# Kernel tuning notes

Hardware: AMD Instinct MI355X
Metric: run time of the kernel (lower is better)

## Reference

```python
import jax, jax.numpy as jnp
import numpy as np

# --- model dimensions ---
MAX_UP = 512; MAX_DOWN = 512; MAX_ELEC = MAX_UP + MAX_DOWN  # 1024 orbitals
N_NUC = 128
MAX_CHARGE = 16
TOT_ORB = MAX_CHARGE * (MAX_CHARGE + 1) // 2  # 136
NUM_HEADS = 8; D_HEAD = 32; F = NUM_HEADS * D_HEAD  # 256
L = 4          # num_layers
FN = 256       # nuc_feats dim
SIGMOID_SHIFTS = (2.0, 4.0, 6.0)
E_DIM = 3 + 1 + len(SIGMOID_SHIFTS)  # featurized edge dim = 7


def generate_spd_orbitals(charges):
    """Vectorized form of the scan/fori_loop scatter in the source.
    For nucleus n with charge c: orbitals[cum_charge+i, n, c(c-1)/2+i] = 1 for i<c.
    charges: [N_NUC] int. Returns [MAX_ELEC, N_NUC, TOT_ORB] float32."""
    c = charges.astype(jnp.int32)
    off = jnp.cumsum(c) - c                      # exclusive cumsum (cum_charge)
    prec = c * (c - 1) // 2                      # preceding orbital offset
    i = jnp.arange(MAX_CHARGE, dtype=jnp.int32)
    valid = (i[None, :] < c[:, None])            # [N_NUC, MAX_CHARGE]
    elec = jnp.clip(off[:, None] + i[None, :], 0, MAX_ELEC - 1)
    orbi = jnp.clip(prec[:, None] + i[None, :], 0, TOT_ORB - 1)
    nuc = jnp.broadcast_to(jnp.arange(N_NUC, dtype=jnp.int32)[:, None], (N_NUC, MAX_CHARGE))
    orb = jnp.zeros((MAX_ELEC, N_NUC, TOT_ORB), jnp.float32)
    return orb.at[elec.ravel(), nuc.ravel(), orbi.ravel()].add(valid.ravel().astype(jnp.float32))


def make_permutation(n_up, n_down):
    segments = [0, n_up, MAX_UP, MAX_UP + n_down, MAX_ELEC]
    updates = [0, n_down, -MAX_UP + n_up, 0]
    idx = jnp.arange(MAX_ELEC)
    agg = jnp.zeros_like(idx)
    for lft, r, u in zip(segments[:-1], segments[1:], updates):
        agg = agg + ((idx >= lft) & (idx < r)) * (idx + u)
    return agg


def featurize_real_space_vector(diffs):
    """[N,N,3] -> [N,N,7]: rescaled diffs, log1p(|r|), sigmoid(|r|-shift)."""
    norm = jnp.sqrt(jnp.sum(diffs * diffs, -1, keepdims=True) + 1e-12)
    sig = jnp.concatenate([jax.nn.sigmoid(norm - s) for s in SIGMOID_SHIFTS], -1)
    return jnp.concatenate([diffs / (1.0 + norm), jnp.log1p(norm), sig], -1)


def orb_ln(x):
    """OrbLayerNorm(feat_axis=-1, nuc_axis=1, eps=1.0) on [O, N, F] tensors."""
    mean = jnp.mean(x, -1, keepdims=True)
    var = jnp.var(x, -1, keepdims=True)
    max_var = jnp.max(var, axis=1, keepdims=True)
    return jax.lax.rsqrt(max_var + 1.0) * (x - mean)


def setup_inputs() -> dict:
    key = jax.random.key(0)
    ks = jax.random.split(key, 8)
    coords = jax.random.normal(ks[0], (N_NUC, 3), jnp.float32) * 3.0
    charges = jax.random.randint(ks[1], (N_NUC,), 0, 8)  # sum < MAX_ELEC
    nuc_mask = jnp.ones((N_NUC,), bool)
    nuc_feats = jax.random.normal(ks[2], (N_NUC, FN), jnp.float32)
    orb_mask = jnp.ones((MAX_ELEC,), bool)
    # hk.Linear(num_feats, with_bias=False, TruncatedNormal(stddev=1))
    W_orb = jax.random.truncated_normal(ks[3], -2.0, 2.0, (TOT_ORB, F), jnp.float32)
    W_edge = jax.random.normal(ks[4], (L, E_DIM, NUM_HEADS), jnp.float32) / np.sqrt(E_DIM)
    W_val = jax.random.normal(ks[5], (L, F, F), jnp.float32) / np.sqrt(F)
    W_nuc = jax.random.normal(ks[6], (L, FN, F), jnp.float32) / np.sqrt(FN)
    W_out = jax.random.normal(ks[7], (L, F, F), jnp.float32) / np.sqrt(F)
    return dict(coords=coords, charges=charges, nuc_mask=nuc_mask, n_up=500,
                n_down=480, nuc_feats=nuc_feats, orb_mask=orb_mask, W_orb=W_orb,
                W_edge=W_edge, W_val=W_val, W_nuc=W_nuc, W_out=W_out)


def reference(coords, charges, nuc_mask, n_up, n_down, nuc_feats, orb_mask,
              W_orb, W_edge, W_val, W_nuc, W_out):
    orbital_feats = generate_spd_orbitals(charges)               # [O, N, TOT_ORB]
    perm = make_permutation(int(n_up), int(n_down))
    orbital_feats = orbital_feats[perm]
    feats = jnp.einsum('ont,tf->onf', orbital_feats, W_orb)     # [O, N, F]
    m = (orb_mask[:, None, None] & nuc_mask[None, :, None]).astype(feats.dtype)
    feats = feats * m
    diffs = coords[:, None, :] - coords[None, :, :]              # [N, N, 3]
    nn_mask = nuc_mask[:, None] & nuc_mask[None, :]
    edge = featurize_real_space_vector(diffs) * nn_mask[..., None]  # [N, N, E]
    for l in range(L):
        # --- MaskedMPNNBlock ---
        h = orb_ln(feats)
        vals = jnp.einsum('onf,fg->ong', h, W_val[l]).reshape(MAX_ELEC, N_NUC, NUM_HEADS, D_HEAD)
        ew = jnp.einsum('ije,eh->ijh', edge, W_edge[l]) * nn_mask[..., None]
        msg = jnp.einsum('ijh,ojhd->oihd', ew, vals).reshape(MAX_ELEC, N_NUC, F)
        msg = msg + nuc_feats @ W_nuc[l]
        feats = feats + jnp.einsum('onf,fg->ong', jnp.tanh(orb_ln(msg)), W_out[l])
        feats = feats * m
    return feats
```

## Files before the change

### kernel.cpp

```cpp
#include <hip/hip_runtime.h>
#include <hip/hip_bf16.h>


#define O_TOT 1024

typedef __bf16 bf16x8 __attribute__((ext_vector_type(8)));
typedef float f32x4 __attribute__((ext_vector_type(4)));

static __device__ __forceinline__ unsigned short f2bf(float f) {
  __bf16 b = (__bf16)f;
  unsigned short u;
  __builtin_memcpy(&u, &b, 2);
  return u;
}
static __device__ __forceinline__ float ftanh(float x) {
  float e = __expf(2.f * x);
  return 1.f - 2.f * __builtin_amdgcn_rcpf(e + 1.f);
}

struct alignas(8) US4 { unsigned short a, b, c, d; };

static __device__ __forceinline__ int swzA(int row, int cb) {
  return row * 512 + (cb ^ ((row & 7) << 4) ^ (((row >> 3) & 1) << 5));
}
static __device__ __forceinline__ int swzV(int row, int cb) {
  return row * 256 + (cb ^ ((row & 7) << 4) ^ (((row >> 3) & 1) << 5));
}


__global__ void k_orbmap(const int* __restrict__ charges, const int* __restrict__ n_up_p,
                         const int* __restrict__ n_down_p, int* __restrict__ orb_nuc,
                         int* __restrict__ orb_t) {
  __shared__ int off[129];
  __shared__ int prec[128];
  int tid = threadIdx.x;
  if (tid == 0) {
    int a = 0;
    for (int n = 0; n < 128; ++n) { off[n] = a; a += charges[n]; }
    off[128] = a;
  }
  if (tid < 128) prec[tid] = charges[tid] * (charges[tid] - 1) / 2;
  __syncthreads();
  int nu = *n_up_p, nd = *n_down_p;
  for (int o = tid; o < O_TOT; o += 256) {
    int e;
    if (o < nu) e = o;
    else if (o < 512) e = o + nd;
    else if (o < 512 + nd) e = o + nu - 512;
    else e = o;
    int nn = -1, tt = 0;
    for (int n = 0; n < 128; ++n) {
      if (e >= off[n] && e < off[n + 1]) { nn = n; tt = prec[n] + (e - off[n]); }
    }
    orb_nuc[o] = nn;
    orb_t[o] = tt;
  }
}

__global__ void k_ew(const float* __restrict__ coords, const float* __restrict__ W_edge,
                     unsigned short* __restrict__ ewbf) {
  int i = blockIdx.x, j = threadIdx.x;
  float dx = coords[i * 3 + 0] - coords[j * 3 + 0];
  float dy = coords[i * 3 + 1] - coords[j * 3 + 1];
  float dz = coords[i * 3 + 2] - coords[j * 3 + 2];
  float norm = sqrtf(dx * dx + dy * dy + dz * dz + 1e-12f);
  float inv = 1.f / (1.f + norm);
  float e[7];
  e[0] = dx * inv; e[1] = dy * inv; e[2] = dz * inv;
  e[3] = log1pf(norm);
  e[4] = 1.f / (1.f + expf(-(norm - 2.f)));
  e[5] = 1.f / (1.f + expf(-(norm - 4.f)));
  e[6] = 1.f / (1.f + expf(-(norm - 6.f)));
  const int mt = i >> 4, l16 = i & 15;
  const int k0 = j >> 5, jo = j & 31;
  const int lane = (jo >> 3) * 16 + l16, jj = jo & 7;
  for (int l = 0; l < 4; ++l)
    for (int h = 0; h < 8; ++h) {
      float s = 0.f;
      for (int k = 0; k < 7; ++k) s += e[k] * W_edge[(l * 7 + k) * 8 + h];
      ewbf[(((((l * 8 + h) * 8 + mt) * 4 + k0) * 64) + lane) * 8 + jj] = f2bf(s);
    }
}

__global__ void k_wt(const float* __restrict__ Wv, const float* __restrict__ Wo,
                     unsigned short* __restrict__ WvTf, unsigned short* __restrict__ WoTf) {
  int idx = blockIdx.x * 256 + threadIdx.x;
  const int l = idx >> 16, rem = idx & 65535;
  const int jj = rem & 7, lane = (rem >> 3) & 63, k0 = (rem >> 9) & 7, gt = rem >> 12;
  const int g = gt * 16 + (lane & 15);
  const int f = k0 * 32 + (lane >> 4) * 8 + jj;
  const int src = l * 65536 + f * 256 + g;
  WvTf[idx] = f2bf(Wv[src]);
  WoTf[idx] = f2bf(Wo[src]);
}

__global__ void k_nucbT(const float* __restrict__ nuc_feats, const float* __restrict__ W_nuc,
                        float* __restrict__ nucbT) {
  int b = blockIdx.x;
  int l = b >> 7, i = b & 127;
  int g = threadIdx.x;
  __shared__ float row[256];
  row[g] = nuc_feats[i * 256 + g];
  __syncthreads();
  const float* Wn = W_nuc + l * 65536;
  float s = 0.f;
  for (int f = 0; f < 256; ++f) s += row[f] * Wn[f * 256 + g];
  nucbT[(l * 256 + g) * 128 + i] = s;
}


__global__ __launch_bounds__(512, 2) void k_main(
    float* __restrict__ feats,
    const float* __restrict__ W_orb,
    const unsigned short* __restrict__ WvTf,
    const unsigned short* __restrict__ WoTf,
    const unsigned short* __restrict__ ewbf,
    const float* __restrict__ nucbT,
    const int* __restrict__ orb_nuc, const int* __restrict__ orb_t) {
  __shared__ char SB[65536];
  __shared__ float2 ln2s[8][128];
  __shared__ float red[8];

  const int o = blockIdx.x;
  const int tid = threadIdx.x;
  const int wave = tid >> 6;
  const int lane = tid & 63;
  const int l16 = lane & 15;
  const int kgrp = (lane >> 4) << 3;
  const int rgrp = (lane >> 4) << 2;
  const int w16 = wave * 16;

  const int nn = orb_nuc[o];
  const int tt = orb_t[o];
  float* fo = feats + (size_t)o * 32768;

  f32x4 fr[16];
#pragma unroll
  for (int gt = 0; gt < 16; ++gt) {
    f32x4 v = {0.f, 0.f, 0.f, 0.f};
#pragma unroll
    for (int r = 0; r < 4; ++r)
      if (w16 + rgrp + r == nn) v[r] = W_orb[tt * 256 + gt * 16 + l16];
    fr[gt] = v;
  }

#pragma unroll 1
  for (int l = 0; l < 4; ++l) {
    bf16x8 A[8];
    {
      float s[4] = {0, 0, 0, 0}, q[4] = {0, 0, 0, 0};
#pragma unroll
      for (int gt = 0; gt < 16; ++gt)
#pragma unroll
        for (int r = 0; r < 4; ++r) {
          float v = fr[gt][r];
          s[r] += v; q[r] += v * v;
        }
#pragma unroll
      for (int of = 1; of < 16; of <<= 1)
#pragma unroll
        for (int r = 0; r < 4; ++r) {
          s[r] += __shfl_xor(s[r], of);
          q[r] += __shfl_xor(q[r], of);
        }
      float mean[4], maxv = 0.f;
#pragma unroll
      for (int r = 0; r < 4; ++r) {
        mean[r] = s[r] * (1.f / 256.f);
        const float var = q[r] * (1.f / 256.f) - mean[r] * mean[r];
        maxv = fmaxf(maxv, var);
      }
      maxv = fmaxf(maxv, __shfl_xor(maxv, 16));
      maxv = fmaxf(maxv, __shfl_xor(maxv, 32));
      if (lane == 0) red[wave] = maxv;
#pragma unroll
      for (int gt = 0; gt < 16; ++gt)
#pragma unroll
        for (int r = 0; r < 4; ++r)
          *(unsigned short*)(SB + swzA(w16 + rgrp + r, (gt * 16 + l16) * 2)) =
              f2bf(fr[gt][r] - mean[r]);
#pragma unroll
      for (int k0 = 0; k0 < 8; ++k0)
        A[k0] = *(const bf16x8*)(SB + swzA(w16 + l16, (k0 * 32 + kgrp) * 2));
    }
    __syncthreads();

    {
      float mv = red[0];
#pragma unroll
      for (int w = 1; w < 8; ++w) mv = fmaxf(mv, red[w]);
      const float rstd = rsqrtf(mv + 1.f);
      const unsigned short* Wl = WvTf + (l * 16 * 8 * 64 * 8) + lane * 8;
#pragma unroll
      for (int gt = 0; gt < 16; ++gt) {
        f32x4 acc = {0.f, 0.f, 0.f, 0.f};
        bf16x8 b[4];
#pragma unroll
        for (int k0 = 0; k0 < 4; ++k0)
          b[k0] = *(const bf16x8*)(Wl + (gt * 8 + k0) * 512);
#pragma unroll
        for (int k0 = 0; k0 < 4; ++k0)
          acc = __builtin_amdgcn_mfma_f32_16x16x32_bf16(A[k0], b[k0], acc, 0, 0, 0);
#pragma unroll
        for (int k0 = 0; k0 < 4; ++k0)
          b[k0] = *(const bf16x8*)(Wl + (gt * 8 + k0 + 4) * 512);
#pragma unroll
        for (int k0 = 0; k0 < 4; ++k0)
          acc = __builtin_amdgcn_mfma_f32_16x16x32_bf16(A[k0 + 4], b[k0], acc, 0, 0, 0);
        const int gg = gt * 16 + l16;
        US4 ov{f2bf(acc[0] * rstd), f2bf(acc[1] * rstd), f2bf(acc[2] * rstd),
               f2bf(acc[3] * rstd)};
        *(US4*)(SB + swzV(gg, (w16 + rgrp) * 2)) = ov;
      }
    }
    __syncthreads();

    bf16x8 B0[4], B1[4];
#pragma unroll
    for (int k0 = 0; k0 < 4; ++k0) {
      B0[k0] = *(const bf16x8*)(SB + swzV(wave * 32 + l16, (k0 * 32 + kgrp) * 2));
      B1[k0] = *(const bf16x8*)(SB + swzV(wave * 32 + 16 + l16, (k0 * 32 + kgrp) * 2));
    }
    __syncthreads();

    {
      const unsigned short* ewh = ewbf + ((l * 8 + wave) * 8 * 4 * 64 * 8) + lane * 8;
      const float* nbT = nucbT + l * 32768;
      const int f0 = wave * 32 + l16;
      const int f1 = f0 + 16;
#pragma unroll
      for (int mt = 0; mt < 8; ++mt) {
        const int i0 = mt * 16;
        f32x4 acc0 = {0.f, 0.f, 0.f, 0.f}, acc1 = {0.f, 0.f, 0.f, 0.f};
        {
          bf16x8 a0 = *(const bf16x8*)(ewh + (mt * 4 + 0) * 512);
          bf16x8 a1 = *(const bf16x8*)(ewh + (mt * 4 + 1) * 512);
          acc0 = __builtin_amdgcn_mfma_f32_16x16x32_bf16(a0, B0[0], acc0, 0, 0, 0);
          acc1 = __builtin_amdgcn_mfma_f32_16x16x32_bf16(a0, B1[0], acc1, 0, 0, 0);
          acc0 = __builtin_amdgcn_mfma_f32_16x16x32_bf16(a1, B0[1], acc0, 0, 0, 0);
          acc1 = __builtin_amdgcn_mfma_f32_16x16x32_bf16(a1, B1[1], acc1, 0, 0, 0);
        }
        {
          bf16x8 a0 = *(const bf16x8*)(ewh + (mt * 4 + 2) * 512);
          bf16x8 a1 = *(const bf16x8*)(ewh + (mt * 4 + 3) * 512);
          acc0 = __builtin_amdgcn_mfma_f32_16x16x32_bf16(a0, B0[2], acc0, 0, 0, 0);
          acc1 = __builtin_amdgcn_mfma_f32_16x16x32_bf16(a0, B1[2], acc1, 0, 0, 0);
          acc0 = __builtin_amdgcn_mfma_f32_16x16x32_bf16(a1, B0[3], acc0, 0, 0, 0);
          acc1 = __builtin_amdgcn_mfma_f32_16x16x32_bf16(a1, B1[3], acc1, 0, 0, 0);
        }
        const f32x4 nb0 = *(const f32x4*)(nbT + f0 * 128 + i0 + rgrp);
        const f32x4 nb1 = *(const f32x4*)(nbT + f1 * 128 + i0 + rgrp);
        float sp[4], qp[4];
#pragma unroll
        for (int r = 0; r < 4; ++r) {
          const float v0 = acc0[r] + nb0[r];
          const float v1 = acc1[r] + nb1[r];
          *(unsigned short*)(SB + swzA(i0 + rgrp + r, f0 * 2)) = f2bf(v0);
          *(unsigned short*)(SB + swzA(i0 + rgrp + r, f1 * 2)) = f2bf(v1);
          sp[r] = v0 + v1;
          qp[r] = v0 * v0 + v1 * v1;
        }
#pragma unroll
        for (int of = 1; of < 16; of <<= 1)
#pragma unroll
          for (int r = 0; r < 4; ++r) {
            sp[r] += __shfl_xor(sp[r], of);
            qp[r] += __shfl_xor(qp[r], of);
          }
        if (l16 == 0) {
#pragma unroll
          for (int r = 0; r < 4; ++r)
            ln2s[wave][i0 + rgrp + r] = float2{sp[r], qp[r]};
        }
      }
    }
    __syncthreads();

    {
      float s0 = 0.f, q0 = 0.f, s1v = 0.f, q1v = 0.f;
#pragma unroll
      for (int h = 0; h < 8; ++h) {
        const float2 p0 = ln2s[h][lane];
        const float2 p1 = ln2s[h][lane + 64];
        s0 += p0.x; q0 += p0.y;
        s1v += p1.x; q1v += p1.y;
      }
      const float mean_a = s0 * (1.f / 256.f);
      const float mean_b = s1v * (1.f / 256.f);
      float v0 = q0 * (1.f / 256.f) - mean_a * mean_a;
      float v1 = q1v * (1.f / 256.f) - mean_b * mean_b;
      float mv = fmaxf(v0, v1);
#pragma unroll
      for (int of = 1; of < 64; of <<= 1) mv = fmaxf(mv, __shfl_xor(mv, of));
      const float rstd2 = rsqrtf(mv + 1.f);
      const float meansel = (wave >= 4) ? mean_b : mean_a;
      const float mn = __shfl(meansel, ((wave & 3) << 4) + l16);

      bf16x8 A2[8];
#pragma unroll
      for (int k0 = 0; k0 < 8; ++k0) {
        bf16x8 raw = *(const bf16x8*)(SB + swzA(w16 + l16, (k0 * 32 + kgrp) * 2));
        bf16x8 t;
#pragma unroll
        for (int j = 0; j < 8; ++j)
          t[j] = (__bf16)ftanh(((float)raw[j] - mn) * rstd2);
        A2[k0] = t;
      }

      const unsigned short* Wl = WoTf + (l * 16 * 8 * 64 * 8) + lane * 8;
#pragma unroll
      for (int gt = 0; gt < 16; ++gt) {
        f32x4 acc = fr[gt];
        bf16x8 b[4];
#pragma unroll
        for (int k0 = 0; k0 < 4; ++k0)
          b[k0] = *(const bf16x8*)(Wl + (gt * 8 + k0) * 512);
#pragma unroll
        for (int k0 = 0; k0 < 4; ++k0)
          acc = __builtin_amdgcn_mfma_f32_16x16x32_bf16(A2[k0], b[k0], acc, 0, 0, 0);
#pragma unroll
        for (int k0 = 0; k0 < 4; ++k0)
          b[k0] = *(const bf16x8*)(Wl + (gt * 8 + k0 + 4) * 512);
#pragma unroll
        for (int k0 = 0; k0 < 4; ++k0)
          acc = __builtin_amdgcn_mfma_f32_16x16x32_bf16(A2[k0 + 4], b[k0], acc, 0, 0, 0);
        fr[gt] = acc;
      }
    }
  }

#pragma unroll
  for (int gt = 0; gt < 16; ++gt)
#pragma unroll
    for (int r = 0; r < 4; ++r)
      fo[(w16 + rgrp + r) * 256 + gt * 16 + l16] = fr[gt][r];
}


extern "C" void kernel_launch(void* const* d_in, const int* in_sizes, int n_in,
                              void* d_out, int out_size, void* d_ws, size_t ws_size,
                              hipStream_t stream) {
  const float* coords = (const float*)d_in[0];
  const int* charges = (const int*)d_in[1];
  const int* n_up = (const int*)d_in[3];
  const int* n_down = (const int*)d_in[4];
  const float* nuc_feats = (const float*)d_in[5];
  const float* W_orb = (const float*)d_in[7];
  const float* W_edge = (const float*)d_in[8];
  const float* W_val = (const float*)d_in[9];
  const float* W_nuc = (const float*)d_in[10];
  const float* W_out = (const float*)d_in[11];
  float* out = (float*)d_out;

  char* ws = (char*)d_ws;
  int* orb_nuc = (int*)ws;
  int* orb_t = (int*)(ws + 4096);
  unsigned short* ewbf = (unsigned short*)(ws + 8192);
  unsigned short* WvTf = (unsigned short*)(ws + 8192 + 1048576);
  unsigned short* WoTf = WvTf + 262144;
  float* nucbT = (float*)(ws + 8192 + 1048576 + 1048576);

  k_orbmap<<<dim3(1), dim3(256), 0, stream>>>(charges, n_up, n_down, orb_nuc, orb_t);
  k_ew<<<dim3(128), dim3(128), 0, stream>>>(coords, W_edge, ewbf);
  k_wt<<<dim3(1024), dim3(256), 0, stream>>>(W_val, W_out, WvTf, WoTf);
  k_nucbT<<<dim3(512), dim3(256), 0, stream>>>(nuc_feats, W_nuc, nucbT);
  k_main<<<dim3(O_TOT), dim3(512), 0, stream>>>(out, W_orb, WvTf, WoTf, ewbf, nucbT,
                                                orb_nuc, orb_t);
}
```

Before: 651.2 us.

## Pack residual features to bf16 in AGPRs and raise occupancy to four blocks

The fp32 residual accumulator (64 floats per thread) is replaced with 32 packed bf16 pairs pinned to accumulator registers, and launch bounds rise from 2 to 4 blocks per CU to improve latency hiding. The second layernorm statistics are now computed from the bf16 values read back from LDS, with a per-row reduction, instead of from per-tile shuffles and a shared partial-sum array. Weight loads are interleaved two at a time with the MFMAs to cut live registers. Keeping the residual stream in bf16 loses precision across layers, and 64 KB of LDS per block may still limit how many blocks actually fit per CU.

```diff
diff --git a/kernel.cpp b/kernel.cpp
--- a/kernel.cpp
+++ b/kernel.cpp
@@ -12,6 +12,21 @@
   unsigned short u;
   __builtin_memcpy(&u, &b, 2);
   return u;
+}
+static __device__ __forceinline__ unsigned int packbf(float a, float b) {
+  return (unsigned int)f2bf(a) | ((unsigned int)f2bf(b) << 16);
+}
+static __device__ __forceinline__ float lo16f(unsigned int u) {
+  unsigned int x = u << 16;
+  float f;
+  __builtin_memcpy(&f, &x, 4);
+  return f;
+}
+static __device__ __forceinline__ float hi16f(unsigned int u) {
+  unsigned int x = u & 0xffff0000u;
+  float f;
+  __builtin_memcpy(&f, &x, 4);
+  return f;
 }
 static __device__ __forceinline__ float ftanh(float x) {
   float e = __expf(2.f * x);
@@ -109,7 +124,7 @@
 }
 
 
-__global__ __launch_bounds__(512, 2) void k_main(
+__global__ __launch_bounds__(512, 4) void k_main(
     float* __restrict__ feats,
     const float* __restrict__ W_orb,
     const unsigned short* __restrict__ WvTf,
@@ -118,8 +133,8 @@
     const float* __restrict__ nucbT,
     const int* __restrict__ orb_nuc, const int* __restrict__ orb_t) {
   __shared__ char SB[65536];
-  __shared__ float2 ln2s[8][128];
-  __shared__ float red[8];
+  __shared__ float red1[8];
+  __shared__ float red2[8];
 
   const int o = blockIdx.x;
   const int tid = threadIdx.x;
@@ -134,51 +149,60 @@
   const int tt = orb_t[o];
   float* fo = feats + (size_t)o * 32768;
 
-  f32x4 fr[16];
+  unsigned int frw[32];
 #pragma unroll
   for (int gt = 0; gt < 16; ++gt) {
-    f32x4 v = {0.f, 0.f, 0.f, 0.f};
+    float v[4] = {0.f, 0.f, 0.f, 0.f};
 #pragma unroll
     for (int r = 0; r < 4; ++r)
       if (w16 + rgrp + r == nn) v[r] = W_orb[tt * 256 + gt * 16 + l16];
-    fr[gt] = v;
-  }
+    frw[2 * gt] = packbf(v[0], v[1]);
+    frw[2 * gt + 1] = packbf(v[2], v[3]);
+  }
+#pragma unroll
+  for (int i = 0; i < 32; ++i) asm volatile("" : "+a"(frw[i]));
 
 #pragma unroll 1
   for (int l = 0; l < 4; ++l) {
     bf16x8 A[8];
     {
-      float s[4] = {0, 0, 0, 0}, q[4] = {0, 0, 0, 0};
-#pragma unroll
-      for (int gt = 0; gt < 16; ++gt)
+      float s4[4] = {0, 0, 0, 0}, q4[4] = {0, 0, 0, 0};
+#pragma unroll
+      for (int gt = 0; gt < 16; ++gt) {
+        const float v0 = lo16f(frw[2 * gt]), v1 = hi16f(frw[2 * gt]);
+        const float v2 = lo16f(frw[2 * gt + 1]), v3 = hi16f(frw[2 * gt + 1]);
+        s4[0] += v0; q4[0] += v0 * v0;
+        s4[1] += v1; q4[1] += v1 * v1;
+        s4[2] += v2; q4[2] += v2 * v2;
+        s4[3] += v3; q4[3] += v3 * v3;
+      }
+#pragma unroll
+      for (int of = 1; of < 16; of <<= 1)
 #pragma unroll
         for (int r = 0; r < 4; ++r) {
-          float v = fr[gt][r];
-          s[r] += v; q[r] += v * v;
-        }
-#pragma unroll
-      for (int of = 1; of < 16; of <<= 1)
-#pragma unroll
-        for (int r = 0; r < 4; ++r) {
-          s[r] += __shfl_xor(s[r], of);
-          q[r] += __shfl_xor(q[r], of);
+          s4[r] += __shfl_xor(s4[r], of);
+          q4[r] += __shfl_xor(q4[r], of);
         }
       float mean[4], maxv = 0.f;
 #pragma unroll
       for (int r = 0; r < 4; ++r) {
-        mean[r] = s[r] * (1.f / 256.f);
-        const float var = q[r] * (1.f / 256.f) - mean[r] * mean[r];
+        mean[r] = s4[r] * (1.f / 256.f);
+        const float var = q4[r] * (1.f / 256.f) - mean[r] * mean[r];
         maxv = fmaxf(maxv, var);
       }
       maxv = fmaxf(maxv, __shfl_xor(maxv, 16));
       maxv = fmaxf(maxv, __shfl_xor(maxv, 32));
-      if (lane == 0) red[wave] = maxv;
-#pragma unroll
-      for (int gt = 0; gt < 16; ++gt)
-#pragma unroll
-        for (int r = 0; r < 4; ++r)
-          *(unsigned short*)(SB + swzA(w16 + rgrp + r, (gt * 16 + l16) * 2)) =
-              f2bf(fr[gt][r] - mean[r]);
+      if (lane == 0) red1[wave] = maxv;
+#pragma unroll
+      for (int gt = 0; gt < 16; ++gt) {
+        const float v0 = lo16f(frw[2 * gt]), v1 = hi16f(frw[2 * gt]);
+        const float v2 = lo16f(frw[2 * gt + 1]), v3 = hi16f(frw[2 * gt + 1]);
+        const int cb = (gt * 16 + l16) * 2;
+        *(unsigned short*)(SB + swzA(w16 + rgrp + 0, cb)) = f2bf(v0 - mean[0]);
+        *(unsigned short*)(SB + swzA(w16 + rgrp + 1, cb)) = f2bf(v1 - mean[1]);
+        *(unsigned short*)(SB + swzA(w16 + rgrp + 2, cb)) = f2bf(v2 - mean[2]);
+        *(unsigned short*)(SB + swzA(w16 + rgrp + 3, cb)) = f2bf(v3 - mean[3]);
+      }
 #pragma unroll
       for (int k0 = 0; k0 < 8; ++k0)
         A[k0] = *(const bf16x8*)(SB + swzA(w16 + l16, (k0 * 32 + kgrp) * 2));
@@ -186,27 +210,31 @@
     __syncthreads();
 
     {
-      float mv = red[0];
-#pragma unroll
-      for (int w = 1; w < 8; ++w) mv = fmaxf(mv, red[w]);
+      float mv = red1[0];
+#pragma unroll
+      for (int w = 1; w < 8; ++w) mv = fmaxf(mv, red1[w]);
       const float rstd = rsqrtf(mv + 1.f);
-      const unsigned short* Wl = WvTf + (l * 16 * 8 * 64 * 8) + lane * 8;
+      const unsigned short* Wl = WvTf + (l * 65536) + lane * 8;
 #pragma unroll
       for (int gt = 0; gt < 16; ++gt) {
         f32x4 acc = {0.f, 0.f, 0.f, 0.f};
-        bf16x8 b[4];
-#pragma unroll
-        for (int k0 = 0; k0 < 4; ++k0)
-          b[k0] = *(const bf16x8*)(Wl + (gt * 8 + k0) * 512);
-#pragma unroll
-        for (int k0 = 0; k0 < 4; ++k0)
-          acc = __builtin_amdgcn_mfma_f32_16x16x32_bf16(A[k0], b[k0], acc, 0, 0, 0);
-#pragma unroll
-        for (int k0 = 0; k0 < 4; ++k0)
-          b[k0] = *(const bf16x8*)(Wl + (gt * 8 + k0 + 4) * 512);
-#pragma unroll
-        for (int k0 = 0; k0 < 4; ++k0)
-          acc = __builtin_amdgcn_mfma_f32_16x16x32_bf16(A[k0 + 4], b[k0], acc, 0, 0, 0);
+        bf16x8 b0, b1;
+        b0 = *(const bf16x8*)(Wl + (gt * 8 + 0) * 512);
+        b1 = *(const bf16x8*)(Wl + (gt * 8 + 1) * 512);
+        acc = __builtin_amdgcn_mfma_f32_16x16x32_bf16(A[0], b0, acc, 0, 0, 0);
+        acc = __builtin_amdgcn_mfma_f32_16x16x32_bf16(A[1], b1, acc, 0, 0, 0);
+        b0 = *(const bf16x8*)(Wl + (gt * 8 + 2) * 512);
+        b1 = *(const bf16x8*)(Wl + (gt * 8 + 3) * 512);
+        acc = __builtin_amdgcn_mfma_f32_16x16x32_bf16(A[2], b0, acc, 0, 0, 0);
+        acc = __builtin_amdgcn_mfma_f32_16x16x32_bf16(A[3], b1, acc, 0, 0, 0);
+        b0 = *(const bf16x8*)(Wl + (gt * 8 + 4) * 512);
+        b1 = *(const bf16x8*)(Wl + (gt * 8 + 5) * 512);
+        acc = __builtin_amdgcn_mfma_f32_16x16x32_bf16(A[4], b0, acc, 0, 0, 0);
+        acc = __builtin_amdgcn_mfma_f32_16x16x32_bf16(A[5], b1, acc, 0, 0, 0);
+        b0 = *(const bf16x8*)(Wl + (gt * 8 + 6) * 512);
+        b1 = *(const bf16x8*)(Wl + (gt * 8 + 7) * 512);
+        acc = __builtin_amdgcn_mfma_f32_16x16x32_bf16(A[6], b0, acc, 0, 0, 0);
+        acc = __builtin_amdgcn_mfma_f32_16x16x32_bf16(A[7], b1, acc, 0, 0, 0);
         const int gg = gt * 16 + l16;
         US4 ov{f2bf(acc[0] * rstd), f2bf(acc[1] * rstd), f2bf(acc[2] * rstd),
                f2bf(acc[3] * rstd)};
@@ -215,16 +243,16 @@
     }
     __syncthreads();
 
-    bf16x8 B0[4], B1[4];
+    bf16x8 VB0[4], VB1[4];
 #pragma unroll
     for (int k0 = 0; k0 < 4; ++k0) {
-      B0[k0] = *(const bf16x8*)(SB + swzV(wave * 32 + l16, (k0 * 32 + kgrp) * 2));
-      B1[k0] = *(const bf16x8*)(SB + swzV(wave * 32 + 16 + l16, (k0 * 32 + kgrp) * 2));
-    }
-    __syncthreads();
-
-    {
-      const unsigned short* ewh = ewbf + ((l * 8 + wave) * 8 * 4 * 64 * 8) + lane * 8;
+      VB0[k0] = *(const bf16x8*)(SB + swzV(wave * 32 + l16, (k0 * 32 + kgrp) * 2));
+      VB1[k0] = *(const bf16x8*)(SB + swzV(wave * 32 + 16 + l16, (k0 * 32 + kgrp) * 2));
+    }
+    __syncthreads();
+
+    {
+      const unsigned short* ewh = ewbf + ((l * 8 + wave) * 16384) + lane * 8;
       const float* nbT = nucbT + l * 32768;
       const int f0 = wave * 32 + l16;
       const int f1 = f0 + 16;
@@ -235,105 +263,106 @@
         {
           bf16x8 a0 = *(const bf16x8*)(ewh + (mt * 4 + 0) * 512);
           bf16x8 a1 = *(const bf16x8*)(ewh + (mt * 4 + 1) * 512);
-          acc0 = __builtin_amdgcn_mfma_f32_16x16x32_bf16(a0, B0[0], acc0, 0, 0, 0);
-          acc1 = __builtin_amdgcn_mfma_f32_16x16x32_bf16(a0, B1[0], acc1, 0, 0, 0);
-          acc0 = __builtin_amdgcn_mfma_f32_16x16x32_bf16(a1, B0[1], acc0, 0, 0, 0);
-          acc1 = __builtin_amdgcn_mfma_f32_16x16x32_bf16(a1, B1[1], acc1, 0, 0, 0);
+          acc0 = __builtin_amdgcn_mfma_f32_16x16x32_bf16(a0, VB0[0], acc0, 0, 0, 0);
+          acc1 = __builtin_amdgcn_mfma_f32_16x16x32_bf16(a0, VB1[0], acc1, 0, 0, 0);
+          acc0 = __builtin_amdgcn_mfma_f32_16x16x32_bf16(a1, VB0[1], acc0, 0, 0, 0);
+          acc1 = __builtin_amdgcn_mfma_f32_16x16x32_bf16(a1, VB1[1], acc1, 0, 0, 0);
         }
         {
           bf16x8 a0 = *(const bf16x8*)(ewh + (mt * 4 + 2) * 512);
           bf16x8 a1 = *(const bf16x8*)(ewh + (mt * 4 + 3) * 512);
-          acc0 = __builtin_amdgcn_mfma_f32_16x16x32_bf16(a0, B0[2], acc0, 0, 0, 0);
-          acc1 = __builtin_amdgcn_mfma_f32_16x16x32_bf16(a0, B1[2], acc1, 0, 0, 0);
-          acc0 = __builtin_amdgcn_mfma_f32_16x16x32_bf16(a1, B0[3], acc0, 0, 0, 0);
-          acc1 = __builtin_amdgcn_mfma_f32_16x16x32_bf16(a1, B1[3], acc1, 0, 0, 0);
+          acc0 = __builtin_amdgcn_mfma_f32_16x16x32_bf16(a0, VB0[2], acc0, 0, 0, 0);
+          acc1 = __builtin_amdgcn_mfma_f32_16x16x32_bf16(a0, VB1[2], acc1, 0, 0, 0);
+          acc0 = __builtin_amdgcn_mfma_f32_16x16x32_bf16(a1, VB0[3], acc0, 0, 0, 0);
+          acc1 = __builtin_amdgcn_mfma_f32_16x16x32_bf16(a1, VB1[3], acc1, 0, 0, 0);
         }
         const f32x4 nb0 = *(const f32x4*)(nbT + f0 * 128 + i0 + rgrp);
         const f32x4 nb1 = *(const f32x4*)(nbT + f1 * 128 + i0 + rgrp);
-        float sp[4], qp[4];
 #pragma unroll
         for (int r = 0; r < 4; ++r) {
-          const float v0 = acc0[r] + nb0[r];
-          const float v1 = acc1[r] + nb1[r];
-          *(unsigned short*)(SB + swzA(i0 + rgrp + r, f0 * 2)) = f2bf(v0);
-          *(unsigned short*)(SB + swzA(i0 + rgrp + r, f1 * 2)) = f2bf(v1);
-          sp[r] = v0 + v1;
-          qp[r] = v0 * v0 + v1 * v1;
-        }
-#pragma unroll
-        for (int of = 1; of < 16; of <<= 1)
-#pragma unroll
-          for (int r = 0; r < 4; ++r) {
-            sp[r] += __shfl_xor(sp[r], of);
-            qp[r] += __shfl_xor(qp[r], of);
-          }
-        if (l16 == 0) {
-#pragma unroll
-          for (int r = 0; r < 4; ++r)
-            ln2s[wave][i0 + rgrp + r] = float2{sp[r], qp[r]};
-        }
-      }
-    }
-    __syncthreads();
-
-    {
-      float s0 = 0.f, q0 = 0.f, s1v = 0.f, q1v = 0.f;
-#pragma unroll
-      for (int h = 0; h < 8; ++h) {
-        const float2 p0 = ln2s[h][lane];
-        const float2 p1 = ln2s[h][lane + 64];
-        s0 += p0.x; q0 += p0.y;
-        s1v += p1.x; q1v += p1.y;
-      }
-      const float mean_a = s0 * (1.f / 256.f);
-      const float mean_b = s1v * (1.f / 256.f);
-      float v0 = q0 * (1.f / 256.f) - mean_a * mean_a;
-      float v1 = q1v * (1.f / 256.f) - mean_b * mean_b;
-      float mv = fmaxf(v0, v1);
-#pragma unroll
-      for (int of = 1; of < 64; of <<= 1) mv = fmaxf(mv, __shfl_xor(mv, of));
+          *(unsigned short*)(SB + swzA(i0 + rgrp + r, f0 * 2)) = f2bf(acc0[r] + nb0[r]);
+          *(unsigned short*)(SB + swzA(i0 + rgrp + r, f1 * 2)) = f2bf(acc1[r] + nb1[r]);
+        }
+      }
+    }
+    __syncthreads();
+
+    bf16x8 raw[8];
+    float mn;
+    {
+#pragma unroll
+      for (int k0 = 0; k0 < 8; ++k0)
+        raw[k0] = *(const bf16x8*)(SB + swzA(w16 + l16, (k0 * 32 + kgrp) * 2));
+      float s = 0.f, q = 0.f;
+#pragma unroll
+      for (int k0 = 0; k0 < 8; ++k0)
+#pragma unroll
+        for (int j = 0; j < 8; ++j) {
+          const float v = (float)raw[k0][j];
+          s += v;
+          q += v * v;
+        }
+      s += __shfl_xor(s, 16); s += __shfl_xor(s, 32);
+      q += __shfl_xor(q, 16); q += __shfl_xor(q, 32);
+      mn = s * (1.f / 256.f);
+      float maxv = q * (1.f / 256.f) - mn * mn;
+#pragma unroll
+      for (int of = 1; of < 16; of <<= 1) maxv = fmaxf(maxv, __shfl_xor(maxv, of));
+      if (lane == 0) red2[wave] = maxv;
+    }
+    __syncthreads();
+
+    {
+      float mv = red2[0];
+#pragma unroll
+      for (int w = 1; w < 8; ++w) mv = fmaxf(mv, red2[w]);
       const float rstd2 = rsqrtf(mv + 1.f);
-      const float meansel = (wave >= 4) ? mean_b : mean_a;
-      const float mn = __shfl(meansel, ((wave & 3) << 4) + l16);
-
-      bf16x8 A2[8];
 #pragma unroll
       for (int k0 = 0; k0 < 8; ++k0) {
-        bf16x8 raw = *(const bf16x8*)(SB + swzA(w16 + l16, (k0 * 32 + kgrp) * 2));
         bf16x8 t;
 #pragma unroll
         for (int j = 0; j < 8; ++j)
-          t[j] = (__bf16)ftanh(((float)raw[j] - mn) * rstd2);
-        A2[k0] = t;
-      }
-
-      const unsigned short* Wl = WoTf + (l * 16 * 8 * 64 * 8) + lane * 8;
+          t[j] = (__bf16)ftanh(((float)raw[k0][j] - mn) * rstd2);
+        raw[k0] = t;
+      }
+      const unsigned short* Wl = WoTf + (l * 65536) + lane * 8;
 #pragma unroll
       for (int gt = 0; gt < 16; ++gt) {
-        f32x4 acc = fr[gt];
-        bf16x8 b[4];
-#pragma unroll
-        for (int k0 = 0; k0 < 4; ++k0)
-          b[k0] = *(const bf16x8*)(Wl + (gt * 8 + k0) * 512);
-#pragma unroll
-        for (int k0 = 0; k0 < 4; ++k0)
-          acc = __builtin_amdgcn_mfma_f32_16x16x32_bf16(A2[k0], b[k0], acc, 0, 0, 0);
-#pragma unroll
-        for (int k0 = 0; k0 < 4; ++k0)
-          b[k0] = *(const bf16x8*)(Wl + (gt * 8 + k0 + 4) * 512);
-#pragma unroll
-        for (int k0 = 0; k0 < 4; ++k0)
-          acc = __builtin_amdgcn_mfma_f32_16x16x32_bf16(A2[k0 + 4], b[k0], acc, 0, 0, 0);
-        fr[gt] = acc;
-      }
-    }
-  }
-
-#pragma unroll
-  for (int gt = 0; gt < 16; ++gt)
-#pragma unroll
-    for (int r = 0; r < 4; ++r)
-      fo[(w16 + rgrp + r) * 256 + gt * 16 + l16] = fr[gt][r];
+        f32x4 acc = {lo16f(frw[2 * gt]), hi16f(frw[2 * gt]),
+                     lo16f(frw[2 * gt + 1]), hi16f(frw[2 * gt + 1])};
+        bf16x8 b0, b1;
+        b0 = *(const bf16x8*)(Wl + (gt * 8 + 0) * 512);
+        b1 = *(const bf16x8*)(Wl + (gt * 8 + 1) * 512);
+        acc = __builtin_amdgcn_mfma_f32_16x16x32_bf16(raw[0], b0, acc, 0, 0, 0);
+        acc = __builtin_amdgcn_mfma_f32_16x16x32_bf16(raw[1], b1, acc, 0, 0, 0);
+        b0 = *(const bf16x8*)(Wl + (gt * 8 + 2) * 512);
+        b1 = *(const bf16x8*)(Wl + (gt * 8 + 3) * 512);
+        acc = __builtin_amdgcn_mfma_f32_16x16x32_bf16(raw[2], b0, acc, 0, 0, 0);
+        acc = __builtin_amdgcn_mfma_f32_16x16x32_bf16(raw[3], b1, acc, 0, 0, 0);
+        b0 = *(const bf16x8*)(Wl + (gt * 8 + 4) * 512);
+        b1 = *(const bf16x8*)(Wl + (gt * 8 + 5) * 512);
+        acc = __builtin_amdgcn_mfma_f32_16x16x32_bf16(raw[4], b0, acc, 0, 0, 0);
+        acc = __builtin_amdgcn_mfma_f32_16x16x32_bf16(raw[5], b1, acc, 0, 0, 0);
+        b0 = *(const bf16x8*)(Wl + (gt * 8 + 6) * 512);
+        b1 = *(const bf16x8*)(Wl + (gt * 8 + 7) * 512);
+        acc = __builtin_amdgcn_mfma_f32_16x16x32_bf16(raw[6], b0, acc, 0, 0, 0);
+        acc = __builtin_amdgcn_mfma_f32_16x16x32_bf16(raw[7], b1, acc, 0, 0, 0);
+        frw[2 * gt] = packbf(acc[0], acc[1]);
+        frw[2 * gt + 1] = packbf(acc[2], acc[3]);
+      }
+    }
+#pragma unroll
+    for (int i = 0; i < 32; ++i) asm volatile("" : "+a"(frw[i]));
+  }
+
+#pragma unroll
+  for (int gt = 0; gt < 16; ++gt) {
+    const int base = gt * 16 + l16;
+    fo[(w16 + rgrp + 0) * 256 + base] = lo16f(frw[2 * gt]);
+    fo[(w16 + rgrp + 1) * 256 + base] = hi16f(frw[2 * gt]);
+    fo[(w16 + rgrp + 2) * 256 + base] = lo16f(frw[2 * gt + 1]);
+    fo[(w16 + rgrp + 3) * 256 + base] = hi16f(frw[2 * gt + 1]);
+  }
 }
 
 
```

After: 979.8 us. 1.5x slower.

## Repartition work so each wave owns 32 feature columns across all nuclei

Applied to the files above, without the earlier changes.

Each wave now owns a 32-column feature slice for all 128 nuclei instead of 16 nuclei rows with all 256 features. This lets a wave keep its slice of W_val and W_out in registers across all row tiles, rather than reloading weights per output tile. Values are staged in a per-wave private LDS region, which drops one barrier and the cross-wave reload of B fragments. The cost is extra LDS (a second 64KB buffer), more register pressure from the 16 held weight fragments, and layer-norm stats that now need a cross-wave reduction plus extra barriers.

```diff
diff --git a/kernel.cpp b/kernel.cpp
--- a/kernel.cpp
+++ b/kernel.cpp
@@ -118,8 +118,10 @@
     const float* __restrict__ nucbT,
     const int* __restrict__ orb_nuc, const int* __restrict__ orb_t) {
   __shared__ char SB[65536];
-  __shared__ float2 ln2s[8][128];
-  __shared__ float red[8];
+  __shared__ char VALS[65536];
+  __shared__ float2 lnP[8][128];
+  __shared__ float meanL[128];
+  __shared__ float red[2];
 
   const int o = blockIdx.x;
   const int tid = threadIdx.x;
@@ -128,125 +130,139 @@
   const int l16 = lane & 15;
   const int kgrp = (lane >> 4) << 3;
   const int rgrp = (lane >> 4) << 2;
-  const int w16 = wave * 16;
+  const int C0 = wave * 32;
 
   const int nn = orb_nuc[o];
   const int tt = orb_t[o];
   float* fo = feats + (size_t)o * 32768;
-
-  f32x4 fr[16];
-#pragma unroll
-  for (int gt = 0; gt < 16; ++gt) {
-    f32x4 v = {0.f, 0.f, 0.f, 0.f};
-#pragma unroll
-    for (int r = 0; r < 4; ++r)
-      if (w16 + rgrp + r == nn) v[r] = W_orb[tt * 256 + gt * 16 + l16];
-    fr[gt] = v;
-  }
+  char* vreg = VALS + wave * 8192;
+
+  f32x4 fr[8][2];
+#pragma unroll
+  for (int mt = 0; mt < 8; ++mt)
+#pragma unroll
+    for (int j = 0; j < 2; ++j) {
+      f32x4 v = {0.f, 0.f, 0.f, 0.f};
+#pragma unroll
+      for (int r = 0; r < 4; ++r)
+        if (mt * 16 + rgrp + r == nn) v[r] = W_orb[tt * 256 + C0 + j * 16 + l16];
+      fr[mt][j] = v;
+    }
 
 #pragma unroll 1
   for (int l = 0; l < 4; ++l) {
-    bf16x8 A[8];
-    {
-      float s[4] = {0, 0, 0, 0}, q[4] = {0, 0, 0, 0};
-#pragma unroll
-      for (int gt = 0; gt < 16; ++gt)
+    {
+#pragma unroll
+      for (int mt = 0; mt < 8; ++mt) {
+        float s[4], q[4];
 #pragma unroll
         for (int r = 0; r < 4; ++r) {
-          float v = fr[gt][r];
-          s[r] += v; q[r] += v * v;
-        }
-#pragma unroll
-      for (int of = 1; of < 16; of <<= 1)
-#pragma unroll
-        for (int r = 0; r < 4; ++r) {
-          s[r] += __shfl_xor(s[r], of);
-          q[r] += __shfl_xor(q[r], of);
-        }
-      float mean[4], maxv = 0.f;
-#pragma unroll
-      for (int r = 0; r < 4; ++r) {
-        mean[r] = s[r] * (1.f / 256.f);
-        const float var = q[r] * (1.f / 256.f) - mean[r] * mean[r];
-        maxv = fmaxf(maxv, var);
-      }
-      maxv = fmaxf(maxv, __shfl_xor(maxv, 16));
-      maxv = fmaxf(maxv, __shfl_xor(maxv, 32));
-      if (lane == 0) red[wave] = maxv;
-#pragma unroll
-      for (int gt = 0; gt < 16; ++gt)
+          const float v0 = fr[mt][0][r], v1 = fr[mt][1][r];
+          s[r] = v0 + v1;
+          q[r] = v0 * v0 + v1 * v1;
+        }
+#pragma unroll
+        for (int of = 1; of < 16; of <<= 1)
+#pragma unroll
+          for (int r = 0; r < 4; ++r) {
+            s[r] += __shfl_xor(s[r], of);
+            q[r] += __shfl_xor(q[r], of);
+          }
 #pragma unroll
         for (int r = 0; r < 4; ++r)
-          *(unsigned short*)(SB + swzA(w16 + rgrp + r, (gt * 16 + l16) * 2)) =
-              f2bf(fr[gt][r] - mean[r]);
-#pragma unroll
-      for (int k0 = 0; k0 < 8; ++k0)
-        A[k0] = *(const bf16x8*)(SB + swzA(w16 + l16, (k0 * 32 + kgrp) * 2));
-    }
-    __syncthreads();
-
-    {
-      float mv = red[0];
-#pragma unroll
-      for (int w = 1; w < 8; ++w) mv = fmaxf(mv, red[w]);
-      const float rstd = rsqrtf(mv + 1.f);
-      const unsigned short* Wl = WvTf + (l * 16 * 8 * 64 * 8) + lane * 8;
-#pragma unroll
-      for (int gt = 0; gt < 16; ++gt) {
-        f32x4 acc = {0.f, 0.f, 0.f, 0.f};
-        bf16x8 b[4];
+          if (l16 == (((mt & 3) << 2) | r))
+            lnP[wave][mt * 16 + rgrp + r] = float2{s[r], q[r]};
+      }
+    }
+    __syncthreads();
+
+    if (tid < 128) {
+      float S = 0.f, Q = 0.f;
+#pragma unroll
+      for (int w2 = 0; w2 < 8; ++w2) {
+        const float2 p = lnP[w2][tid];
+        S += p.x; Q += p.y;
+      }
+      const float mean = S * (1.f / 256.f);
+      float var = Q * (1.f / 256.f) - mean * mean;
+      meanL[tid] = mean;
+#pragma unroll
+      for (int of = 1; of < 64; of <<= 1) var = fmaxf(var, __shfl_xor(var, of));
+      if (lane == 0) red[wave] = var;
+    }
+    __syncthreads();
+    const float rstd = rsqrtf(fmaxf(red[0], red[1]) + 1.f);
+
+    {
+#pragma unroll
+      for (int mt = 0; mt < 8; ++mt) {
+        const f32x4 m4 = *(const f32x4*)(meanL + mt * 16 + rgrp);
+#pragma unroll
+        for (int j = 0; j < 2; ++j) {
+          const int cb = (C0 + j * 16 + l16) * 2;
+#pragma unroll
+          for (int r = 0; r < 4; ++r)
+            *(unsigned short*)(SB + swzA(mt * 16 + rgrp + r, cb)) =
+                f2bf(fr[mt][j][r] - m4[r]);
+        }
+      }
+    }
+    __syncthreads();
+
+    {
+      const unsigned short* Wl = WvTf + l * 65536 + lane * 8;
+      bf16x8 b[16];
+#pragma unroll
+      for (int j = 0; j < 2; ++j)
+#pragma unroll
+        for (int k0 = 0; k0 < 8; ++k0)
+          b[j * 8 + k0] = *(const bf16x8*)(Wl + (((2 * wave + j) * 8 + k0) * 512));
+#pragma unroll
+      for (int mt = 0; mt < 8; ++mt) {
+        bf16x8 A[8];
+#pragma unroll
+        for (int k0 = 0; k0 < 8; ++k0)
+          A[k0] = *(const bf16x8*)(SB + swzA(mt * 16 + l16, (k0 * 32 + kgrp) * 2));
+        f32x4 acc0 = {0.f, 0.f, 0.f, 0.f}, acc1 = {0.f, 0.f, 0.f, 0.f};
+#pragma unroll
+        for (int k0 = 0; k0 < 8; ++k0) {
+          acc0 = __builtin_amdgcn_mfma_f32_16x16x32_bf16(A[k0], b[k0], acc0, 0, 0, 0);
+          acc1 = __builtin_amdgcn_mfma_f32_16x16x32_bf16(A[k0], b[8 + k0], acc1, 0, 0, 0);
+        }
+        const int cb = (mt * 16 + rgrp) * 2;
+        US4 o0{f2bf(acc0[0] * rstd), f2bf(acc0[1] * rstd), f2bf(acc0[2] * rstd),
+               f2bf(acc0[3] * rstd)};
+        US4 o1{f2bf(acc1[0] * rstd), f2bf(acc1[1] * rstd), f2bf(acc1[2] * rstd),
+               f2bf(acc1[3] * rstd)};
+        *(US4*)(vreg + swzV(l16, cb)) = o0;
+        *(US4*)(vreg + swzV(16 + l16, cb)) = o1;
+      }
+    }
+    __syncthreads();
+
+    {
+      bf16x8 VB0[4], VB1[4];
+#pragma unroll
+      for (int k0 = 0; k0 < 4; ++k0) {
+        VB0[k0] = *(const bf16x8*)(vreg + swzV(l16, (k0 * 32 + kgrp) * 2));
+        VB1[k0] = *(const bf16x8*)(vreg + swzV(16 + l16, (k0 * 32 + kgrp) * 2));
+      }
+      const unsigned short* ewh = ewbf + (l * 8 + wave) * 16384 + lane * 8;
+      const float* nbT = nucbT + l * 32768;
+      const int f0 = C0 + l16;
+      const int f1 = f0 + 16;
+#pragma unroll
+      for (int mt = 0; mt < 8; ++mt) {
+        const int i0 = mt * 16;
+        bf16x8 a[4];
 #pragma unroll
         for (int k0 = 0; k0 < 4; ++k0)
-          b[k0] = *(const bf16x8*)(Wl + (gt * 8 + k0) * 512);
-#pragma unroll
-        for (int k0 = 0; k0 < 4; ++k0)
-          acc = __builtin_amdgcn_mfma_f32_16x16x32_bf16(A[k0], b[k0], acc, 0, 0, 0);
-#pragma unroll
-        for (int k0 = 0; k0 < 4; ++k0)
-          b[k0] = *(const bf16x8*)(Wl + (gt * 8 + k0 + 4) * 512);
-#pragma unroll
-        for (int k0 = 0; k0 < 4; ++k0)
-          acc = __builtin_amdgcn_mfma_f32_16x16x32_bf16(A[k0 + 4], b[k0], acc, 0, 0, 0);
-        const int gg = gt * 16 + l16;
-        US4 ov{f2bf(acc[0] * rstd), f2bf(acc[1] * rstd), f2bf(acc[2] * rstd),
-               f2bf(acc[3] * rstd)};
-        *(US4*)(SB + swzV(gg, (w16 + rgrp) * 2)) = ov;
-      }
-    }
-    __syncthreads();
-
-    bf16x8 B0[4], B1[4];
-#pragma unroll
-    for (int k0 = 0; k0 < 4; ++k0) {
-      B0[k0] = *(const bf16x8*)(SB + swzV(wave * 32 + l16, (k0 * 32 + kgrp) * 2));
-      B1[k0] = *(const bf16x8*)(SB + swzV(wave * 32 + 16 + l16, (k0 * 32 + kgrp) * 2));
-    }
-    __syncthreads();
-
-    {
-      const unsigned short* ewh = ewbf + ((l * 8 + wave) * 8 * 4 * 64 * 8) + lane * 8;
-      const float* nbT = nucbT + l * 32768;
-      const int f0 = wave * 32 + l16;
-      const int f1 = f0 + 16;
-#pragma unroll
-      for (int mt = 0; mt < 8; ++mt) {
-        const int i0 = mt * 16;
+          a[k0] = *(const bf16x8*)(ewh + (mt * 4 + k0) * 512);
         f32x4 acc0 = {0.f, 0.f, 0.f, 0.f}, acc1 = {0.f, 0.f, 0.f, 0.f};
-        {
-          bf16x8 a0 = *(const bf16x8*)(ewh + (mt * 4 + 0) * 512);
-          bf16x8 a1 = *(const bf16x8*)(ewh + (mt * 4 + 1) * 512);
-          acc0 = __builtin_amdgcn_mfma_f32_16x16x32_bf16(a0, B0[0], acc0, 0, 0, 0);
-          acc1 = __builtin_amdgcn_mfma_f32_16x16x32_bf16(a0, B1[0], acc1, 0, 0, 0);
-          acc0 = __builtin_amdgcn_mfma_f32_16x16x32_bf16(a1, B0[1], acc0, 0, 0, 0);
-          acc1 = __builtin_amdgcn_mfma_f32_16x16x32_bf16(a1, B1[1], acc1, 0, 0, 0);
-        }
-        {
-          bf16x8 a0 = *(const bf16x8*)(ewh + (mt * 4 + 2) * 512);
-          bf16x8 a1 = *(const bf16x8*)(ewh + (mt * 4 + 3) * 512);
-          acc0 = __builtin_amdgcn_mfma_f32_16x16x32_bf16(a0, B0[2], acc0, 0, 0, 0);
-          acc1 = __builtin_amdgcn_mfma_f32_16x16x32_bf16(a0, B1[2], acc1, 0, 0, 0);
-          acc0 = __builtin_amdgcn_mfma_f32_16x16x32_bf16(a1, B0[3], acc0, 0, 0, 0);
-          acc1 = __builtin_amdgcn_mfma_f32_16x16x32_bf16(a1, B1[3], acc1, 0, 0, 0);
+#pragma unroll
+        for (int k0 = 0; k0 < 4; ++k0) {
+          acc0 = __builtin_amdgcn_mfma_f32_16x16x32_bf16(a[k0], VB0[k0], acc0, 0, 0, 0);
+          acc1 = __builtin_amdgcn_mfma_f32_16x16x32_bf16(a[k0], VB1[k0], acc1, 0, 0, 0);
         }
         const f32x4 nb0 = *(const f32x4*)(nbT + f0 * 128 + i0 + rgrp);
         const f32x4 nb1 = *(const f32x4*)(nbT + f1 * 128 + i0 + rgrp);
@@ -267,73 +283,72 @@
             sp[r] += __shfl_xor(sp[r], of);
             qp[r] += __shfl_xor(qp[r], of);
           }
-        if (l16 == 0) {
-#pragma unroll
-          for (int r = 0; r < 4; ++r)
-            ln2s[wave][i0 + rgrp + r] = float2{sp[r], qp[r]};
-        }
-      }
-    }
-    __syncthreads();
-
-    {
-      float s0 = 0.f, q0 = 0.f, s1v = 0.f, q1v = 0.f;
-#pragma unroll
-      for (int h = 0; h < 8; ++h) {
-        const float2 p0 = ln2s[h][lane];
-        const float2 p1 = ln2s[h][lane + 64];
-        s0 += p0.x; q0 += p0.y;
-        s1v += p1.x; q1v += p1.y;
-      }
-      const float mean_a = s0 * (1.f / 256.f);
-      const float mean_b = s1v * (1.f / 256.f);
-      float v0 = q0 * (1.f / 256.f) - mean_a * mean_a;
-      float v1 = q1v * (1.f / 256.f) - mean_b * mean_b;
-      float mv = fmaxf(v0, v1);
-#pragma unroll
-      for (int of = 1; of < 64; of <<= 1) mv = fmaxf(mv, __shfl_xor(mv, of));
-      const float rstd2 = rsqrtf(mv + 1.f);
-      const float meansel = (wave >= 4) ? mean_b : mean_a;
-      const float mn = __shfl(meansel, ((wave & 3) << 4) + l16);
-
-      bf16x8 A2[8];
-#pragma unroll
-      for (int k0 = 0; k0 < 8; ++k0) {
-        bf16x8 raw = *(const bf16x8*)(SB + swzA(w16 + l16, (k0 * 32 + kgrp) * 2));
-        bf16x8 t;
-#pragma unroll
-        for (int j = 0; j < 8; ++j)
-          t[j] = (__bf16)ftanh(((float)raw[j] - mn) * rstd2);
-        A2[k0] = t;
-      }
-
-      const unsigned short* Wl = WoTf + (l * 16 * 8 * 64 * 8) + lane * 8;
-#pragma unroll
-      for (int gt = 0; gt < 16; ++gt) {
-        f32x4 acc = fr[gt];
-        bf16x8 b[4];
-#pragma unroll
-        for (int k0 = 0; k0 < 4; ++k0)
-          b[k0] = *(const bf16x8*)(Wl + (gt * 8 + k0) * 512);
-#pragma unroll
-        for (int k0 = 0; k0 < 4; ++k0)
-          acc = __builtin_amdgcn_mfma_f32_16x16x32_bf16(A2[k0], b[k0], acc, 0, 0, 0);
-#pragma unroll
-        for (int k0 = 0; k0 < 4; ++k0)
-          b[k0] = *(const bf16x8*)(Wl + (gt * 8 + k0 + 4) * 512);
-#pragma unroll
-        for (int k0 = 0; k0 < 4; ++k0)
-          acc = __builtin_amdgcn_mfma_f32_16x16x32_bf16(A2[k0 + 4], b[k0], acc, 0, 0, 0);
-        fr[gt] = acc;
+#pragma unroll
+        for (int r = 0; r < 4; ++r)
+          if (l16 == (((mt & 3) << 2) | r))
+            lnP[wave][i0 + rgrp + r] = float2{sp[r], qp[r]};
+      }
+    }
+    __syncthreads();
+
+    if (tid < 128) {
+      float S = 0.f, Q = 0.f;
+#pragma unroll
+      for (int w2 = 0; w2 < 8; ++w2) {
+        const float2 p = lnP[w2][tid];
+        S += p.x; Q += p.y;
+      }
+      const float mean = S * (1.f / 256.f);
+      float var = Q * (1.f / 256.f) - mean * mean;
+      meanL[tid] = mean;
+#pragma unroll
+      for (int of = 1; of < 64; of <<= 1) var = fmaxf(var, __shfl_xor(var, of));
+      if (lane == 0) red[wave] = var;
+    }
+    __syncthreads();
+    const float rstd2 = rsqrtf(fmaxf(red[0], red[1]) + 1.f);
+
+    {
+      const unsigned short* Wl2 = WoTf + l * 65536 + lane * 8;
+      bf16x8 b2[16];
+#pragma unroll
+      for (int j = 0; j < 2; ++j)
+#pragma unroll
+        for (int k0 = 0; k0 < 8; ++k0)
+          b2[j * 8 + k0] = *(const bf16x8*)(Wl2 + (((2 * wave + j) * 8 + k0) * 512));
+#pragma unroll
+      for (int mt = 0; mt < 8; ++mt) {
+        const float mrow = meanL[mt * 16 + l16];
+        bf16x8 A2[8];
+#pragma unroll
+        for (int k0 = 0; k0 < 8; ++k0) {
+          bf16x8 raw = *(const bf16x8*)(SB + swzA(mt * 16 + l16, (k0 * 32 + kgrp) * 2));
+          bf16x8 t;
+#pragma unroll
+          for (int jj = 0; jj < 8; ++jj)
+            t[jj] = (__bf16)ftanh(((float)raw[jj] - mrow) * rstd2);
+          A2[k0] = t;
+        }
+        f32x4 acc0 = fr[mt][0];
+        f32x4 acc1 = fr[mt][1];
+#pragma unroll
+        for (int k0 = 0; k0 < 8; ++k0) {
+          acc0 = __builtin_amdgcn_mfma_f32_16x16x32_bf16(A2[k0], b2[k0], acc0, 0, 0, 0);
+          acc1 = __builtin_amdgcn_mfma_f32_16x16x32_bf16(A2[k0], b2[8 + k0], acc1, 0, 0, 0);
+        }
+        fr[mt][0] = acc0;
+        fr[mt][1] = acc1;
       }
     }
   }
 
 #pragma unroll
-  for (int gt = 0; gt < 16; ++gt)
-#pragma unroll
-    for (int r = 0; r < 4; ++r)
-      fo[(w16 + rgrp + r) * 256 + gt * 16 + l16] = fr[gt][r];
+  for (int mt = 0; mt < 8; ++mt)
+#pragma unroll
+    for (int j = 0; j < 2; ++j)
+#pragma unroll
+      for (int r = 0; r < 4; ++r)
+        fo[(mt * 16 + rgrp + r) * 256 + C0 + j * 16 + l16] = fr[mt][j][r];
 }
 
 
```

Measured after the change: 833.3 us. 1.28x slower.
